# Performance work log

Hardware: AMD Instinct MI355X
Metric: run time of the kernel (lower is better)

The kernel has to match this reference:

```python
import jax, jax.numpy as jnp
import numpy as np

W_SZ = 5          # fine_window_size
D_F = 128         # fine d_model
D_C = 256         # coarse d_model


def _unfold(x, W, stride):
    # x: [B, C, H, Wd] -> [B, L, W*W, C], matching torch F.unfold + reshape/permute
    B, C, H, Wd = x.shape
    p = W // 2
    xp = jnp.pad(x, ((0, 0), (0, 0), (p, p), (p, p)))
    Hc = (H + 2 * p - W) // stride + 1
    Wc = (Wd + 2 * p - W) // stride + 1
    ri = (jnp.arange(Hc) * stride)[:, None] + jnp.arange(W)          # [Hc, W]
    ci = (jnp.arange(Wc) * stride)[:, None] + jnp.arange(W)          # [Wc, W]
    # gather -> [B, C, Hc, W, Wc, W]
    patches = xp[:, :, ri[:, :, None, None], ci[None, None, :, :]]
    # -> [B, Hc, Wc, W, W, C] -> [B, L, W*W, C]
    patches = patches.transpose(0, 2, 4, 3, 5, 1)
    return patches.reshape(B, Hc * Wc, W * W, C)


def setup_inputs() -> dict:
    key = jax.random.key(0)
    ks = jax.random.split(key, 10)
    B, Hf, Wf = 2, 240, 320
    L = 4800  # 60*80 coarse cells
    M = 3000
    inp = {
        "feat_f0": jax.random.normal(ks[0], (B, D_F, Hf, Wf), jnp.float32),
        "feat_f1": jax.random.normal(ks[1], (B, D_F, Hf, Wf), jnp.float32),
        "feat_c0": jax.random.normal(ks[2], (B, L, D_C), jnp.float32),
        "feat_c1": jax.random.normal(ks[3], (B, L, D_C), jnp.float32),
        "hw0_f": 240,
        "hw0_c": 60,
        "b_ids": jax.random.randint(ks[4], (M,), 0, B, jnp.int64 if jax.config.jax_enable_x64 else jnp.int32),
        "i_ids": jax.random.randint(ks[5], (M,), 0, L, jnp.int64 if jax.config.jax_enable_x64 else jnp.int32),
        "j_ids": jax.random.randint(ks[6], (M,), 0, L, jnp.int64 if jax.config.jax_enable_x64 else jnp.int32),
        # Linear params, torch convention: y = x @ W.T + b
        "down_W": jax.random.normal(ks[7], (D_F, D_C), jnp.float32) * (2.0 / D_C) ** 0.5,
        "down_b": jnp.zeros((D_F,), jnp.float32),
        "merge_W": jax.random.normal(ks[8], (D_F, 2 * D_F), jnp.float32) * (1.0 / D_F) ** 0.5,
        "merge_b": jnp.zeros((D_F,), jnp.float32),
    }
    return inp


def reference(feat_f0, feat_f1, feat_c0, feat_c1, hw0_f, hw0_c,
              b_ids, i_ids, j_ids, down_W, down_b, merge_W, merge_b):
    W = W_SZ
    stride = hw0_f // hw0_c  # python int -> static
    # unfold both fine maps -> [B, L, W^2, d_f]
    f0_unf = _unfold(feat_f0, W, stride)
    f1_unf = _unfold(feat_f1, W, stride)
    # gather per-match windows -> [M, W^2, d_f]
    f0_win = f0_unf[b_ids, i_ids]
    f1_win = f1_unf[b_ids, j_ids]
    # coarse feats per match, concat along match dim -> [2M, d_c]
    c_cat = jnp.concatenate([feat_c0[b_ids, i_ids], feat_c1[b_ids, j_ids]], axis=0)
    c_win = c_cat @ down_W.T + down_b                                   # [2M, d_f]
    f_cat = jnp.concatenate([f0_win, f1_win], axis=0)                   # [2M, W^2, d_f]
    c_rep = jnp.broadcast_to(c_win[:, None, :], f_cat.shape)            # [2M, W^2, d_f]
    merged = jnp.concatenate([f_cat, c_rep], axis=-1) @ merge_W.T + merge_b
    M = b_ids.shape[0]
    return merged[:M], merged[M:]
```

## Files before the change

### kernel.cpp

```cpp
#include <hip/hip_runtime.h>


#define HF 240
#define WF 320
#define HWF (HF * WF)
#define LPOS 4800

typedef short short8 __attribute__((ext_vector_type(8)));
typedef unsigned short ushort8 __attribute__((ext_vector_type(8)));
typedef float f32x4 __attribute__((ext_vector_type(4)));

__device__ __forceinline__ unsigned short f2bf(float x) {
  union { float f; unsigned u; } v; v.f = x;
  unsigned r = v.u + 0x7FFF + ((v.u >> 16) & 1);
  return (unsigned short)(r >> 16);
}

__global__ __launch_bounds__(256) void transpose_kernel(
    const float* __restrict__ f0, const float* __restrict__ f1,
    unsigned short* __restrict__ t0, unsigned short* __restrict__ t1) {
  const int t = threadIdx.x;
  const int px = blockIdx.x * 256 + t;
  const int c8 = blockIdx.y;
  const int mb = blockIdx.z;
  const float* src = ((mb >> 1) ? f1 : f0)
                   + ((size_t)(mb & 1) * 128 + (size_t)c8 * 8) * HWF + px;
  unsigned short* dst = ((mb >> 1) ? t1 : t0)
                      + (((size_t)(mb & 1) * 16 + (size_t)c8) * HWF + px) * 8;

  float v[8];
  #pragma unroll
  for (int j = 0; j < 8; ++j) v[j] = src[(size_t)j * HWF];
  ushort8 u;
  #pragma unroll
  for (int j = 0; j < 8; ++j) u[j] = f2bf(v[j]);
  *(ushort8*)dst = u;
}

__global__ __launch_bounds__(256) void prep_kernel(
    const float* __restrict__ down_W, const float* __restrict__ down_b,
    const float* __restrict__ merge_W, const float* __restrict__ merge_b,
    float* __restrict__ CW, float* __restrict__ cbias,
    unsigned short* __restrict__ W1bf) {
  int idx = blockIdx.x * 256 + threadIdx.x;
  if (idx < 32768) {
    int k = idx >> 7, o = idx & 127;
    float s = 0.f;
    #pragma unroll 4
    for (int t = 0; t < 128; ++t)
      s += down_W[t * 256 + k] * merge_W[o * 256 + 128 + t];
    CW[idx] = s;
  } else if (idx < 49152) {
    int i2 = idx - 32768;
    int n = i2 >> 7, c = i2 & 127;
    W1bf[i2] = f2bf(merge_W[n * 256 + c]);
  } else if (idx < 49280) {
    int o = idx - 49152;
    float s = merge_b[o];
    #pragma unroll 4
    for (int t = 0; t < 128; ++t)
      s += down_b[t] * merge_W[o * 256 + 128 + t];
    cbias[o] = s;
  }
}

__global__ __launch_bounds__(256) void t2_kernel(
    const float* __restrict__ c0, const float* __restrict__ c1,
    const int* __restrict__ b_ids, const int* __restrict__ i_ids,
    const int* __restrict__ j_ids,
    const float* __restrict__ CW, const float* __restrict__ cbias,
    float* __restrict__ t2, int M) {
  __shared__ float crow[8][256];
  const int t = threadIdx.x;
  const int m0 = blockIdx.x * 8;
  const int M2 = 2 * M;
  #pragma unroll
  for (int it = 0; it < 8; ++it) {
    int m = m0 + it;
    float v = 0.f;
    if (m < M2) {
      int b, pos;
      const float* src;
      if (m < M) { b = b_ids[m]; pos = i_ids[m]; src = c0; }
      else       { b = b_ids[m - M]; pos = j_ids[m - M]; src = c1; }
      v = src[((size_t)b * LPOS + pos) * 256 + t];
    }
    crow[it][t] = v;
  }
  __syncthreads();
  const int o = t & 127, half = t >> 7;
  const int r0 = half * 4;
  float a0 = 0.f, a1 = 0.f, a2 = 0.f, a3 = 0.f;
  #pragma unroll 4
  for (int k = 0; k < 256; ++k) {
    float wv = CW[k * 128 + o];
    a0 += crow[r0 + 0][k] * wv;
    a1 += crow[r0 + 1][k] * wv;
    a2 += crow[r0 + 2][k] * wv;
    a3 += crow[r0 + 3][k] * wv;
  }
  const float cb = cbias[o];
  if (m0 + r0 + 0 < M2) t2[(size_t)(m0 + r0 + 0) * 128 + o] = a0 + cb;
  if (m0 + r0 + 1 < M2) t2[(size_t)(m0 + r0 + 1) * 128 + o] = a1 + cb;
  if (m0 + r0 + 2 < M2) t2[(size_t)(m0 + r0 + 2) * 128 + o] = a2 + cb;
  if (m0 + r0 + 3 < M2) t2[(size_t)(m0 + r0 + 3) * 128 + o] = a3 + cb;
}

__global__ __launch_bounds__(256) void fine_mfma_kernel(
    const unsigned short* __restrict__ t0, const unsigned short* __restrict__ t1,
    const int* __restrict__ b_ids, const int* __restrict__ i_ids,
    const int* __restrict__ j_ids,
    const unsigned short* __restrict__ W1bf, const float* __restrict__ t2,
    float* __restrict__ out, int M) {
  __shared__ unsigned short Bl[128 * 128];
  const int t = threadIdx.x;

  #pragma unroll
  for (int it = 0; it < 8; ++it) {
    int q = it * 256 + t;
    int n = q >> 4;
    int kb16 = (q & 15) * 16;
    short8 v = *(const short8*)&W1bf[n * 128 + (q & 15) * 8];
    int dstB = n * 256 + (kb16 ^ ((n & 7) << 4));
    *(short8*)((char*)Bl + dstB) = v;
  }

  const int wid = t >> 6, lane = t & 63;
  const int lr = lane & 15, lg = lane >> 4;
  const int m = blockIdx.x * 4 + wid;
  const int M2 = 2 * M;
  const bool active = (m < M2);

  short8 a[2][4];
  short8 az = {};
  if (active) {
    int b, pos;
    const unsigned short* tm;
    if (m < M) { b = b_ids[m]; pos = i_ids[m]; tm = t0; }
    else       { int mm = m - M; b = b_ids[mm]; pos = j_ids[mm]; tm = t1; }
    tm += (size_t)b * 16 * HWF * 8;
    int hc = pos / 80, wc = pos - hc * 80;
    int h0 = hc * 4 - 2, w0 = wc * 4 - 2;
    #pragma unroll
    for (int mt = 0; mt < 2; ++mt) {
      int p = mt * 16 + lr;
      int pr = p / 5;
      int hh = h0 + pr, ww = w0 + (p - pr * 5);
      bool valid = (p < 25) && ((unsigned)hh < (unsigned)HF) && ((unsigned)ww < (unsigned)WF);
      int px = valid ? (hh * WF + ww) : 0;
      #pragma unroll
      for (int kk = 0; kk < 4; ++kk) {
        const short8* ap =
            (const short8*)(tm + (((size_t)(kk * 4 + lg) * HWF + px) << 3));
        a[mt][kk] = valid ? *ap : az;
      }
    }
  } else {
    #pragma unroll
    for (int mt = 0; mt < 2; ++mt)
      #pragma unroll
      for (int kk = 0; kk < 4; ++kk) a[mt][kk] = az;
  }

  __syncthreads();
  if (!active) return;

  f32x4 acc[2][8];
  #pragma unroll
  for (int mt = 0; mt < 2; ++mt)
    #pragma unroll
    for (int nt = 0; nt < 8; ++nt) {
      f32x4 z = {0.f, 0.f, 0.f, 0.f};
      acc[mt][nt] = z;
    }

  #pragma unroll
  for (int nt = 0; nt < 8; ++nt) {
    int n = nt * 16 + lr;
    int kbase = n * 256;
    int sw = (n & 7) << 4;
    short8 bfr[4];
    #pragma unroll
    for (int kk = 0; kk < 4; ++kk) {
      int kb = (kk * 64 + lg * 16) ^ sw;
      bfr[kk] = *(const short8*)((const char*)Bl + kbase + kb);
    }
    #pragma unroll
    for (int kk = 0; kk < 4; ++kk) {
      acc[0][nt] = __builtin_amdgcn_mfma_f32_16x16x32_bf16(a[0][kk], bfr[kk], acc[0][nt], 0, 0, 0);
      acc[1][nt] = __builtin_amdgcn_mfma_f32_16x16x32_bf16(a[1][kk], bfr[kk], acc[1][nt], 0, 0, 0);
    }
  }

  const float* t2row = t2 + (size_t)m * 128;
  float* orow = out + (size_t)m * 25 * 128;
  #pragma unroll
  for (int nt = 0; nt < 8; ++nt) {
    int o = nt * 16 + lr;
    float tv = t2row[o];
    #pragma unroll
    for (int mt = 0; mt < 2; ++mt) {
      #pragma unroll
      for (int j = 0; j < 4; ++j) {
        int r = mt * 16 + lg * 4 + j;
        if (r < 25) orow[r * 128 + o] = acc[mt][nt][j] + tv;
      }
    }
  }
}

extern "C" void kernel_launch(void* const* d_in, const int* in_sizes, int n_in,
                              void* d_out, int out_size, void* d_ws, size_t ws_size,
                              hipStream_t stream) {
  const float* f0      = (const float*)d_in[0];
  const float* f1      = (const float*)d_in[1];
  const float* c0      = (const float*)d_in[2];
  const float* c1      = (const float*)d_in[3];
  const int*   b_ids   = (const int*)d_in[6];
  const int*   i_ids   = (const int*)d_in[7];
  const int*   j_ids   = (const int*)d_in[8];
  const float* down_W  = (const float*)d_in[9];
  const float* down_b  = (const float*)d_in[10];
  const float* merge_W = (const float*)d_in[11];
  const float* merge_b = (const float*)d_in[12];
  const int M = in_sizes[6];
  const int M2 = 2 * M;

  char* wsb = (char*)d_ws;
  float* CW    = (float*)wsb;
  float* cbias = (float*)(wsb + 131072);
  float* t2    = (float*)(wsb + 131584);
  size_t off = 131584 + (size_t)M2 * 128 * 4;
  off = (off + 255) & ~(size_t)255;
  unsigned short* W1bf = (unsigned short*)(wsb + off);
  off += 32768;
  unsigned short* t0 = (unsigned short*)(wsb + off);
  off += (size_t)2 * 16 * HWF * 8 * 2;
  unsigned short* t1 = (unsigned short*)(wsb + off);

  transpose_kernel<<<dim3(300, 16, 4), 256, 0, stream>>>(f0, f1, t0, t1);
  prep_kernel<<<193, 256, 0, stream>>>(down_W, down_b, merge_W, merge_b,
                                       CW, cbias, W1bf);
  t2_kernel<<<(M2 + 7) / 8, 256, 0, stream>>>(c0, c1, b_ids, i_ids, j_ids,
                                              CW, cbias, t2, M);
  fine_mfma_kernel<<<(M2 + 3) / 4, 256, 0, stream>>>(t0, t1, b_ids, i_ids, j_ids,
                                                     W1bf, t2, (float*)d_out, M);
}
```

Measured before the change: 107.0 us.

## Gather fine windows directly from NCHW fp32 and drop the transpose pass

Removes the kernel that converted both full fine feature maps into a channel-blocked bf16 layout. The MFMA kernel now reads the 5x5 window pixels straight from the original fp32 NCHW tensors with per-channel strided loads and converts them to bf16 in registers. This avoids reading and rewriting the whole feature maps when only a small set of windows is used. In exchange, the gather is much less coalesced: each element is a scattered 4-byte load rather than a 16-byte vector load.

```diff
diff --git a/kernel.cpp b/kernel.cpp
--- a/kernel.cpp
+++ b/kernel.cpp
@@ -7,34 +7,12 @@
 #define LPOS 4800
 
 typedef short short8 __attribute__((ext_vector_type(8)));
-typedef unsigned short ushort8 __attribute__((ext_vector_type(8)));
 typedef float f32x4 __attribute__((ext_vector_type(4)));
 
 __device__ __forceinline__ unsigned short f2bf(float x) {
   union { float f; unsigned u; } v; v.f = x;
   unsigned r = v.u + 0x7FFF + ((v.u >> 16) & 1);
   return (unsigned short)(r >> 16);
-}
-
-__global__ __launch_bounds__(256) void transpose_kernel(
-    const float* __restrict__ f0, const float* __restrict__ f1,
-    unsigned short* __restrict__ t0, unsigned short* __restrict__ t1) {
-  const int t = threadIdx.x;
-  const int px = blockIdx.x * 256 + t;
-  const int c8 = blockIdx.y;
-  const int mb = blockIdx.z;
-  const float* src = ((mb >> 1) ? f1 : f0)
-                   + ((size_t)(mb & 1) * 128 + (size_t)c8 * 8) * HWF + px;
-  unsigned short* dst = ((mb >> 1) ? t1 : t0)
-                      + (((size_t)(mb & 1) * 16 + (size_t)c8) * HWF + px) * 8;
-
-  float v[8];
-  #pragma unroll
-  for (int j = 0; j < 8; ++j) v[j] = src[(size_t)j * HWF];
-  ushort8 u;
-  #pragma unroll
-  for (int j = 0; j < 8; ++j) u[j] = f2bf(v[j]);
-  *(ushort8*)dst = u;
 }
 
 __global__ __launch_bounds__(256) void prep_kernel(
@@ -107,7 +85,7 @@
 }
 
 __global__ __launch_bounds__(256) void fine_mfma_kernel(
-    const unsigned short* __restrict__ t0, const unsigned short* __restrict__ t1,
+    const float* __restrict__ f0, const float* __restrict__ f1,
     const int* __restrict__ b_ids, const int* __restrict__ i_ids,
     const int* __restrict__ j_ids,
     const unsigned short* __restrict__ W1bf, const float* __restrict__ t2,
@@ -132,13 +110,17 @@
   const bool active = (m < M2);
 
   short8 a[2][4];
-  short8 az = {};
+  #pragma unroll
+  for (int mt = 0; mt < 2; ++mt)
+    #pragma unroll
+    for (int kk = 0; kk < 4; ++kk) a[mt][kk] = (short8){};
+
   if (active) {
     int b, pos;
-    const unsigned short* tm;
-    if (m < M) { b = b_ids[m]; pos = i_ids[m]; tm = t0; }
-    else       { int mm = m - M; b = b_ids[mm]; pos = j_ids[mm]; tm = t1; }
-    tm += (size_t)b * 16 * HWF * 8;
+    const float* src;
+    if (m < M) { b = b_ids[m]; pos = i_ids[m]; src = f0; }
+    else       { int mm = m - M; b = b_ids[mm]; pos = j_ids[mm]; src = f1; }
+    const float* base = src + (size_t)b * 128 * HWF;
     int hc = pos / 80, wc = pos - hc * 80;
     int h0 = hc * 4 - 2, w0 = wc * 4 - 2;
     #pragma unroll
@@ -147,19 +129,19 @@
       int pr = p / 5;
       int hh = h0 + pr, ww = w0 + (p - pr * 5);
       bool valid = (p < 25) && ((unsigned)hh < (unsigned)HF) && ((unsigned)ww < (unsigned)WF);
-      int px = valid ? (hh * WF + ww) : 0;
+      const float* ap = base + (valid ? (hh * WF + ww) : 0) + (size_t)lg * 8 * HWF;
       #pragma unroll
       for (int kk = 0; kk < 4; ++kk) {
-        const short8* ap =
-            (const short8*)(tm + (((size_t)(kk * 4 + lg) * HWF + px) << 3));
-        a[mt][kk] = valid ? *ap : az;
+        float v[8];
+        #pragma unroll
+        for (int j = 0; j < 8; ++j)
+          v[j] = valid ? ap[((size_t)kk * 32 + j) * HWF] : 0.f;
+        short8 fr;
+        #pragma unroll
+        for (int j = 0; j < 8; ++j) fr[j] = (short)f2bf(v[j]);
+        a[mt][kk] = fr;
       }
     }
-  } else {
-    #pragma unroll
-    for (int mt = 0; mt < 2; ++mt)
-      #pragma unroll
-      for (int kk = 0; kk < 4; ++kk) a[mt][kk] = az;
   }
 
   __syncthreads();
@@ -233,16 +215,11 @@
   size_t off = 131584 + (size_t)M2 * 128 * 4;
   off = (off + 255) & ~(size_t)255;
   unsigned short* W1bf = (unsigned short*)(wsb + off);
-  off += 32768;
-  unsigned short* t0 = (unsigned short*)(wsb + off);
-  off += (size_t)2 * 16 * HWF * 8 * 2;
-  unsigned short* t1 = (unsigned short*)(wsb + off);
-
-  transpose_kernel<<<dim3(300, 16, 4), 256, 0, stream>>>(f0, f1, t0, t1);
+
   prep_kernel<<<193, 256, 0, stream>>>(down_W, down_b, merge_W, merge_b,
                                        CW, cbias, W1bf);
   t2_kernel<<<(M2 + 7) / 8, 256, 0, stream>>>(c0, c1, b_ids, i_ids, j_ids,
                                               CW, cbias, t2, M);
-  fine_mfma_kernel<<<(M2 + 3) / 4, 256, 0, stream>>>(t0, t1, b_ids, i_ids, j_ids,
+  fine_mfma_kernel<<<(M2 + 3) / 4, 256, 0, stream>>>(f0, f1, b_ids, i_ids, j_ids,
                                                      W1bf, t2, (float*)d_out, M);
 }
```

Result: slower. 143.0 us (+33.6%).

## Merge transpose into t2 kernel and process two matches per wave in MFMA kernel

Applied to the files above, without the earlier changes.

The fp32-to-bf16 channel-packing transpose now runs as extra blocks of the t2 projection kernel, which removes one launch and lets the two independent jobs overlap. The transposed output is written with nontemporal stores. The fine MFMA kernel now loops over two matches per wave, so each staged copy of the bf16 weight in shared memory is reused across eight matches instead of four. The cost is a serial loop inside each wave and half as many blocks, which lowers parallelism and latency hiding for the gather loads.

```diff
diff --git a/kernel.cpp b/kernel.cpp
--- a/kernel.cpp
+++ b/kernel.cpp
@@ -14,27 +14,6 @@
   union { float f; unsigned u; } v; v.f = x;
   unsigned r = v.u + 0x7FFF + ((v.u >> 16) & 1);
   return (unsigned short)(r >> 16);
-}
-
-__global__ __launch_bounds__(256) void transpose_kernel(
-    const float* __restrict__ f0, const float* __restrict__ f1,
-    unsigned short* __restrict__ t0, unsigned short* __restrict__ t1) {
-  const int t = threadIdx.x;
-  const int px = blockIdx.x * 256 + t;
-  const int c8 = blockIdx.y;
-  const int mb = blockIdx.z;
-  const float* src = ((mb >> 1) ? f1 : f0)
-                   + ((size_t)(mb & 1) * 128 + (size_t)c8 * 8) * HWF + px;
-  unsigned short* dst = ((mb >> 1) ? t1 : t0)
-                      + (((size_t)(mb & 1) * 16 + (size_t)c8) * HWF + px) * 8;
-
-  float v[8];
-  #pragma unroll
-  for (int j = 0; j < 8; ++j) v[j] = src[(size_t)j * HWF];
-  ushort8 u;
-  #pragma unroll
-  for (int j = 0; j < 8; ++j) u[j] = f2bf(v[j]);
-  *(ushort8*)dst = u;
 }
 
 __global__ __launch_bounds__(256) void prep_kernel(
@@ -64,15 +43,39 @@
   }
 }
 
-__global__ __launch_bounds__(256) void t2_kernel(
+__global__ __launch_bounds__(256) void work_kernel(
+    const float* __restrict__ f0, const float* __restrict__ f1,
+    unsigned short* __restrict__ t0, unsigned short* __restrict__ t1,
     const float* __restrict__ c0, const float* __restrict__ c1,
     const int* __restrict__ b_ids, const int* __restrict__ i_ids,
     const int* __restrict__ j_ids,
     const float* __restrict__ CW, const float* __restrict__ cbias,
-    float* __restrict__ t2, int M) {
+    float* __restrict__ t2, int M, int T2B) {
   __shared__ float crow[8][256];
   const int t = threadIdx.x;
-  const int m0 = blockIdx.x * 8;
+  const int bid = blockIdx.x;
+
+  if (bid >= T2B) {
+    const int q = bid - T2B;
+    const int bx = q % 300;
+    const int c8 = (q / 300) & 15;
+    const int mb = q / 4800;
+    const int px = bx * 256 + t;
+    const float* src = ((mb >> 1) ? f1 : f0)
+                     + ((size_t)(mb & 1) * 128 + (size_t)c8 * 8) * HWF + px;
+    unsigned short* dst = ((mb >> 1) ? t1 : t0)
+                        + (((size_t)(mb & 1) * 16 + (size_t)c8) * HWF + px) * 8;
+    float v[8];
+    #pragma unroll
+    for (int j = 0; j < 8; ++j) v[j] = src[(size_t)j * HWF];
+    ushort8 u;
+    #pragma unroll
+    for (int j = 0; j < 8; ++j) u[j] = f2bf(v[j]);
+    __builtin_nontemporal_store(u, (ushort8*)dst);
+    return;
+  }
+
+  const int m0 = bid * 8;
   const int M2 = 2 * M;
   #pragma unroll
   for (int it = 0; it < 8; ++it) {
@@ -124,86 +127,83 @@
     int dstB = n * 256 + (kb16 ^ ((n & 7) << 4));
     *(short8*)((char*)Bl + dstB) = v;
   }
+  __syncthreads();
 
   const int wid = t >> 6, lane = t & 63;
   const int lr = lane & 15, lg = lane >> 4;
-  const int m = blockIdx.x * 4 + wid;
   const int M2 = 2 * M;
-  const bool active = (m < M2);
-
-  short8 a[2][4];
-  short8 az = {};
-  if (active) {
-    int b, pos;
-    const unsigned short* tm;
-    if (m < M) { b = b_ids[m]; pos = i_ids[m]; tm = t0; }
-    else       { int mm = m - M; b = b_ids[mm]; pos = j_ids[mm]; tm = t1; }
-    tm += (size_t)b * 16 * HWF * 8;
-    int hc = pos / 80, wc = pos - hc * 80;
-    int h0 = hc * 4 - 2, w0 = wc * 4 - 2;
-    #pragma unroll
-    for (int mt = 0; mt < 2; ++mt) {
-      int p = mt * 16 + lr;
-      int pr = p / 5;
-      int hh = h0 + pr, ww = w0 + (p - pr * 5);
-      bool valid = (p < 25) && ((unsigned)hh < (unsigned)HF) && ((unsigned)ww < (unsigned)WF);
-      int px = valid ? (hh * WF + ww) : 0;
+
+  #pragma unroll 1
+  for (int im = 0; im < 2; ++im) {
+    const int m = blockIdx.x * 8 + im * 4 + wid;
+    if (m >= M2) continue;
+
+    short8 a[2][4];
+    short8 az = {};
+    {
+      int b, pos;
+      const unsigned short* tm;
+      if (m < M) { b = b_ids[m]; pos = i_ids[m]; tm = t0; }
+      else       { int mm = m - M; b = b_ids[mm]; pos = j_ids[mm]; tm = t1; }
+      tm += (size_t)b * 16 * HWF * 8;
+      int hc = pos / 80, wc = pos - hc * 80;
+      int h0 = hc * 4 - 2, w0 = wc * 4 - 2;
+      #pragma unroll
+      for (int mt = 0; mt < 2; ++mt) {
+        int p = mt * 16 + lr;
+        int pr = p / 5;
+        int hh = h0 + pr, ww = w0 + (p - pr * 5);
+        bool valid = (p < 25) && ((unsigned)hh < (unsigned)HF) && ((unsigned)ww < (unsigned)WF);
+        int px = valid ? (hh * WF + ww) : 0;
+        #pragma unroll
+        for (int kk = 0; kk < 4; ++kk) {
+          const short8* ap =
+              (const short8*)(tm + (((size_t)(kk * 4 + lg) * HWF + px) << 3));
+          a[mt][kk] = valid ? *ap : az;
+        }
+      }
+    }
+
+    f32x4 acc[2][8];
+    #pragma unroll
+    for (int mt = 0; mt < 2; ++mt)
+      #pragma unroll
+      for (int nt = 0; nt < 8; ++nt) {
+        f32x4 z = {0.f, 0.f, 0.f, 0.f};
+        acc[mt][nt] = z;
+      }
+
+    #pragma unroll
+    for (int nt = 0; nt < 8; ++nt) {
+      int n = nt * 16 + lr;
+      int kbase = n * 256;
+      int sw = (n & 7) << 4;
+      short8 bfr[4];
       #pragma unroll
       for (int kk = 0; kk < 4; ++kk) {
-        const short8* ap =
-            (const short8*)(tm + (((size_t)(kk * 4 + lg) * HWF + px) << 3));
-        a[mt][kk] = valid ? *ap : az;
-      }
-    }
-  } else {
-    #pragma unroll
-    for (int mt = 0; mt < 2; ++mt)
-      #pragma unroll
-      for (int kk = 0; kk < 4; ++kk) a[mt][kk] = az;
-  }
-
-  __syncthreads();
-  if (!active) return;
-
-  f32x4 acc[2][8];
-  #pragma unroll
-  for (int mt = 0; mt < 2; ++mt)
+        int kb = (kk * 64 + lg * 16) ^ sw;
+        bfr[kk] = *(const short8*)((const char*)Bl + kbase + kb);
+      }
+      #pragma unroll
+      for (int kk = 0; kk < 4; ++kk) {
+        acc[0][nt] = __builtin_amdgcn_mfma_f32_16x16x32_bf16(a[0][kk], bfr[kk], acc[0][nt], 0, 0, 0);
+        acc[1][nt] = __builtin_amdgcn_mfma_f32_16x16x32_bf16(a[1][kk], bfr[kk], acc[1][nt], 0, 0, 0);
+      }
+    }
+
+    const float* t2row = t2 + (size_t)m * 128;
+    float* orow = out + (size_t)m * 25 * 128;
     #pragma unroll
     for (int nt = 0; nt < 8; ++nt) {
-      f32x4 z = {0.f, 0.f, 0.f, 0.f};
-      acc[mt][nt] = z;
-    }
-
-  #pragma unroll
-  for (int nt = 0; nt < 8; ++nt) {
-    int n = nt * 16 + lr;
-    int kbase = n * 256;
-    int sw = (n & 7) << 4;
-    short8 bfr[4];
-    #pragma unroll
-    for (int kk = 0; kk < 4; ++kk) {
-      int kb = (kk * 64 + lg * 16) ^ sw;
-      bfr[kk] = *(const short8*)((const char*)Bl + kbase + kb);
-    }
-    #pragma unroll
-    for (int kk = 0; kk < 4; ++kk) {
-      acc[0][nt] = __builtin_amdgcn_mfma_f32_16x16x32_bf16(a[0][kk], bfr[kk], acc[0][nt], 0, 0, 0);
-      acc[1][nt] = __builtin_amdgcn_mfma_f32_16x16x32_bf16(a[1][kk], bfr[kk], acc[1][nt], 0, 0, 0);
-    }
-  }
-
-  const float* t2row = t2 + (size_t)m * 128;
-  float* orow = out + (size_t)m * 25 * 128;
-  #pragma unroll
-  for (int nt = 0; nt < 8; ++nt) {
-    int o = nt * 16 + lr;
-    float tv = t2row[o];
-    #pragma unroll
-    for (int mt = 0; mt < 2; ++mt) {
-      #pragma unroll
-      for (int j = 0; j < 4; ++j) {
-        int r = mt * 16 + lg * 4 + j;
-        if (r < 25) orow[r * 128 + o] = acc[mt][nt][j] + tv;
+      int o = nt * 16 + lr;
+      float tv = t2row[o];
+      #pragma unroll
+      for (int mt = 0; mt < 2; ++mt) {
+        #pragma unroll
+        for (int j = 0; j < 4; ++j) {
+          int r = mt * 16 + lg * 4 + j;
+          if (r < 25) orow[r * 128 + o] = acc[mt][nt][j] + tv;
+        }
       }
     }
   }
@@ -225,6 +225,7 @@
   const float* merge_b = (const float*)d_in[12];
   const int M = in_sizes[6];
   const int M2 = 2 * M;
+  const int T2B = (M2 + 7) / 8;
 
   char* wsb = (char*)d_ws;
   float* CW    = (float*)wsb;
@@ -238,11 +239,11 @@
   off += (size_t)2 * 16 * HWF * 8 * 2;
   unsigned short* t1 = (unsigned short*)(wsb + off);
 
-  transpose_kernel<<<dim3(300, 16, 4), 256, 0, stream>>>(f0, f1, t0, t1);
   prep_kernel<<<193, 256, 0, stream>>>(down_W, down_b, merge_W, merge_b,
                                        CW, cbias, W1bf);
-  t2_kernel<<<(M2 + 7) / 8, 256, 0, stream>>>(c0, c1, b_ids, i_ids, j_ids,
-                                              CW, cbias, t2, M);
-  fine_mfma_kernel<<<(M2 + 3) / 4, 256, 0, stream>>>(t0, t1, b_ids, i_ids, j_ids,
+  work_kernel<<<T2B + 19200, 256, 0, stream>>>(f0, f1, t0, t1, c0, c1,
+                                               b_ids, i_ids, j_ids,
+                                               CW, cbias, t2, M, T2B);
+  fine_mfma_kernel<<<(M2 + 7) / 8, 256, 0, stream>>>(t0, t1, b_ids, i_ids, j_ids,
                                                      W1bf, t2, (float*)d_out, M);
 }
```

After: 99.23 us (median of 2 runs). 1.08x faster.

## Fuse coarse projection into fine MFMA kernel and use nontemporal transpose stores

Applied to the files above, without the earlier changes.

Merges the coarse-feature projection (t2) kernel into the fine MFMA kernel. Each block now handles 8 matches, computes their projected coarse rows into shared memory, then each wave processes two matches in sequence. This removes one kernel launch and the global round trip of the t2 buffer, and spreads the W1 shared-memory load over twice as many matches. The transpose kernel now uses nontemporal stores and is launched after prep. The cost is more shared memory per block and half as many blocks, with serialized work inside each wave.

```diff
diff --git a/kernel.cpp b/kernel.cpp
--- a/kernel.cpp
+++ b/kernel.cpp
@@ -34,7 +34,7 @@
   ushort8 u;
   #pragma unroll
   for (int j = 0; j < 8; ++j) u[j] = f2bf(v[j]);
-  *(ushort8*)dst = u;
+  __builtin_nontemporal_store(u, (ushort8*)dst);
 }
 
 __global__ __launch_bounds__(256) void prep_kernel(
@@ -64,56 +64,19 @@
   }
 }
 
-__global__ __launch_bounds__(256) void t2_kernel(
+__global__ __launch_bounds__(256) void fine_mfma_kernel(
+    const unsigned short* __restrict__ t0, const unsigned short* __restrict__ t1,
     const float* __restrict__ c0, const float* __restrict__ c1,
     const int* __restrict__ b_ids, const int* __restrict__ i_ids,
     const int* __restrict__ j_ids,
+    const unsigned short* __restrict__ W1bf,
     const float* __restrict__ CW, const float* __restrict__ cbias,
-    float* __restrict__ t2, int M) {
-  __shared__ float crow[8][256];
-  const int t = threadIdx.x;
-  const int m0 = blockIdx.x * 8;
-  const int M2 = 2 * M;
-  #pragma unroll
-  for (int it = 0; it < 8; ++it) {
-    int m = m0 + it;
-    float v = 0.f;
-    if (m < M2) {
-      int b, pos;
-      const float* src;
-      if (m < M) { b = b_ids[m]; pos = i_ids[m]; src = c0; }
-      else       { b = b_ids[m - M]; pos = j_ids[m - M]; src = c1; }
-      v = src[((size_t)b * LPOS + pos) * 256 + t];
-    }
-    crow[it][t] = v;
-  }
-  __syncthreads();
-  const int o = t & 127, half = t >> 7;
-  const int r0 = half * 4;
-  float a0 = 0.f, a1 = 0.f, a2 = 0.f, a3 = 0.f;
-  #pragma unroll 4
-  for (int k = 0; k < 256; ++k) {
-    float wv = CW[k * 128 + o];
-    a0 += crow[r0 + 0][k] * wv;
-    a1 += crow[r0 + 1][k] * wv;
-    a2 += crow[r0 + 2][k] * wv;
-    a3 += crow[r0 + 3][k] * wv;
-  }
-  const float cb = cbias[o];
-  if (m0 + r0 + 0 < M2) t2[(size_t)(m0 + r0 + 0) * 128 + o] = a0 + cb;
-  if (m0 + r0 + 1 < M2) t2[(size_t)(m0 + r0 + 1) * 128 + o] = a1 + cb;
-  if (m0 + r0 + 2 < M2) t2[(size_t)(m0 + r0 + 2) * 128 + o] = a2 + cb;
-  if (m0 + r0 + 3 < M2) t2[(size_t)(m0 + r0 + 3) * 128 + o] = a3 + cb;
-}
-
-__global__ __launch_bounds__(256) void fine_mfma_kernel(
-    const unsigned short* __restrict__ t0, const unsigned short* __restrict__ t1,
-    const int* __restrict__ b_ids, const int* __restrict__ i_ids,
-    const int* __restrict__ j_ids,
-    const unsigned short* __restrict__ W1bf, const float* __restrict__ t2,
     float* __restrict__ out, int M) {
   __shared__ unsigned short Bl[128 * 128];
+  __shared__ float crow[8][256];
+  __shared__ float t2l[8][128];
   const int t = threadIdx.x;
+  const int M2 = 2 * M;
 
   #pragma unroll
   for (int it = 0; it < 8; ++it) {
@@ -125,85 +88,116 @@
     *(short8*)((char*)Bl + dstB) = v;
   }
 
+  const int m0 = blockIdx.x * 8;
+  #pragma unroll
+  for (int it = 0; it < 8; ++it) {
+    int m = m0 + it;
+    float v = 0.f;
+    if (m < M2) {
+      int b, pos;
+      const float* srcc;
+      if (m < M) { b = b_ids[m]; pos = i_ids[m]; srcc = c0; }
+      else       { b = b_ids[m - M]; pos = j_ids[m - M]; srcc = c1; }
+      v = srcc[((size_t)b * LPOS + pos) * 256 + t];
+    }
+    crow[it][t] = v;
+  }
+  __syncthreads();
+
+  {
+    const int o = t & 127, half = t >> 7;
+    const int r0 = half * 4;
+    float a0 = 0.f, a1 = 0.f, a2 = 0.f, a3 = 0.f;
+    #pragma unroll 4
+    for (int k = 0; k < 256; ++k) {
+      float wv = CW[k * 128 + o];
+      a0 += crow[r0 + 0][k] * wv;
+      a1 += crow[r0 + 1][k] * wv;
+      a2 += crow[r0 + 2][k] * wv;
+      a3 += crow[r0 + 3][k] * wv;
+    }
+    const float cb = cbias[o];
+    t2l[r0 + 0][o] = a0 + cb;
+    t2l[r0 + 1][o] = a1 + cb;
+    t2l[r0 + 2][o] = a2 + cb;
+    t2l[r0 + 3][o] = a3 + cb;
+  }
+  __syncthreads();
+
   const int wid = t >> 6, lane = t & 63;
   const int lr = lane & 15, lg = lane >> 4;
-  const int m = blockIdx.x * 4 + wid;
-  const int M2 = 2 * M;
-  const bool active = (m < M2);
-
-  short8 a[2][4];
-  short8 az = {};
-  if (active) {
-    int b, pos;
-    const unsigned short* tm;
-    if (m < M) { b = b_ids[m]; pos = i_ids[m]; tm = t0; }
-    else       { int mm = m - M; b = b_ids[mm]; pos = j_ids[mm]; tm = t1; }
-    tm += (size_t)b * 16 * HWF * 8;
-    int hc = pos / 80, wc = pos - hc * 80;
-    int h0 = hc * 4 - 2, w0 = wc * 4 - 2;
-    #pragma unroll
-    for (int mt = 0; mt < 2; ++mt) {
-      int p = mt * 16 + lr;
-      int pr = p / 5;
-      int hh = h0 + pr, ww = w0 + (p - pr * 5);
-      bool valid = (p < 25) && ((unsigned)hh < (unsigned)HF) && ((unsigned)ww < (unsigned)WF);
-      int px = valid ? (hh * WF + ww) : 0;
-      #pragma unroll
-      for (int kk = 0; kk < 4; ++kk) {
-        const short8* ap =
-            (const short8*)(tm + (((size_t)(kk * 4 + lg) * HWF + px) << 3));
-        a[mt][kk] = valid ? *ap : az;
-      }
-    }
-  } else {
+
+  #pragma unroll 1
+  for (int im = 0; im < 2; ++im) {
+    const int mrow = im * 4 + wid;
+    const int m = m0 + mrow;
+    if (m >= M2) continue;
+
+    short8 a[2][4];
+    short8 az = {};
+    {
+      int b, pos;
+      const unsigned short* tm;
+      if (m < M) { b = b_ids[m]; pos = i_ids[m]; tm = t0; }
+      else       { int mm = m - M; b = b_ids[mm]; pos = j_ids[mm]; tm = t1; }
+      tm += (size_t)b * 16 * HWF * 8;
+      int hc = pos / 80, wc = pos - hc * 80;
+      int h0 = hc * 4 - 2, w0 = wc * 4 - 2;
+      #pragma unroll
+      for (int mt = 0; mt < 2; ++mt) {
+        int p = mt * 16 + lr;
+        int pr = p / 5;
+        int hh = h0 + pr, ww = w0 + (p - pr * 5);
+        bool valid = (p < 25) && ((unsigned)hh < (unsigned)HF) && ((unsigned)ww < (unsigned)WF);
+        int px = valid ? (hh * WF + ww) : 0;
+        #pragma unroll
+        for (int kk = 0; kk < 4; ++kk) {
+          const short8* ap =
+              (const short8*)(tm + (((size_t)(kk * 4 + lg) * HWF + px) << 3));
+          a[mt][kk] = valid ? *ap : az;
+        }
+      }
+    }
+
+    f32x4 acc[2][8];
     #pragma unroll
     for (int mt = 0; mt < 2; ++mt)
       #pragma unroll
-      for (int kk = 0; kk < 4; ++kk) a[mt][kk] = az;
-  }
-
-  __syncthreads();
-  if (!active) return;
-
-  f32x4 acc[2][8];
-  #pragma unroll
-  for (int mt = 0; mt < 2; ++mt)
+      for (int nt = 0; nt < 8; ++nt) {
+        f32x4 z = {0.f, 0.f, 0.f, 0.f};
+        acc[mt][nt] = z;
+      }
+
     #pragma unroll
     for (int nt = 0; nt < 8; ++nt) {
-      f32x4 z = {0.f, 0.f, 0.f, 0.f};
-      acc[mt][nt] = z;
-    }
-
-  #pragma unroll
-  for (int nt = 0; nt < 8; ++nt) {
-    int n = nt * 16 + lr;
-    int kbase = n * 256;
-    int sw = (n & 7) << 4;
-    short8 bfr[4];
+      int n = nt * 16 + lr;
+      int kbase = n * 256;
+      int sw = (n & 7) << 4;
+      short8 bfr[4];
+      #pragma unroll
+      for (int kk = 0; kk < 4; ++kk) {
+        int kb = (kk * 64 + lg * 16) ^ sw;
+        bfr[kk] = *(const short8*)((const char*)Bl + kbase + kb);
+      }
+      #pragma unroll
+      for (int kk = 0; kk < 4; ++kk) {
+        acc[0][nt] = __builtin_amdgcn_mfma_f32_16x16x32_bf16(a[0][kk], bfr[kk], acc[0][nt], 0, 0, 0);
+        acc[1][nt] = __builtin_amdgcn_mfma_f32_16x16x32_bf16(a[1][kk], bfr[kk], acc[1][nt], 0, 0, 0);
+      }
+    }
+
+    float* orow = out + (size_t)m * 25 * 128;
     #pragma unroll
-    for (int kk = 0; kk < 4; ++kk) {
-      int kb = (kk * 64 + lg * 16) ^ sw;
-      bfr[kk] = *(const short8*)((const char*)Bl + kbase + kb);
-    }
-    #pragma unroll
-    for (int kk = 0; kk < 4; ++kk) {
-      acc[0][nt] = __builtin_amdgcn_mfma_f32_16x16x32_bf16(a[0][kk], bfr[kk], acc[0][nt], 0, 0, 0);
-      acc[1][nt] = __builtin_amdgcn_mfma_f32_16x16x32_bf16(a[1][kk], bfr[kk], acc[1][nt], 0, 0, 0);
-    }
-  }
-
-  const float* t2row = t2 + (size_t)m * 128;
-  float* orow = out + (size_t)m * 25 * 128;
-  #pragma unroll
-  for (int nt = 0; nt < 8; ++nt) {
-    int o = nt * 16 + lr;
-    float tv = t2row[o];
-    #pragma unroll
-    for (int mt = 0; mt < 2; ++mt) {
-      #pragma unroll
-      for (int j = 0; j < 4; ++j) {
-        int r = mt * 16 + lg * 4 + j;
-        if (r < 25) orow[r * 128 + o] = acc[mt][nt][j] + tv;
+    for (int nt = 0; nt < 8; ++nt) {
+      int o = nt * 16 + lr;
+      float tv = t2l[mrow][o];
+      #pragma unroll
+      for (int mt = 0; mt < 2; ++mt) {
+        #pragma unroll
+        for (int j = 0; j < 4; ++j) {
+          int r = mt * 16 + lg * 4 + j;
+          if (r < 25) orow[r * 128 + o] = acc[mt][nt][j] + tv;
+        }
       }
     }
   }
@@ -229,8 +223,7 @@
   char* wsb = (char*)d_ws;
   float* CW    = (float*)wsb;
   float* cbias = (float*)(wsb + 131072);
-  float* t2    = (float*)(wsb + 131584);
-  size_t off = 131584 + (size_t)M2 * 128 * 4;
+  size_t off = 131584;
   off = (off + 255) & ~(size_t)255;
   unsigned short* W1bf = (unsigned short*)(wsb + off);
   off += 32768;
@@ -238,11 +231,11 @@
   off += (size_t)2 * 16 * HWF * 8 * 2;
   unsigned short* t1 = (unsigned short*)(wsb + off);
 
-  transpose_kernel<<<dim3(300, 16, 4), 256, 0, stream>>>(f0, f1, t0, t1);
   prep_kernel<<<193, 256, 0, stream>>>(down_W, down_b, merge_W, merge_b,
                                        CW, cbias, W1bf);
-  t2_kernel<<<(M2 + 7) / 8, 256, 0, stream>>>(c0, c1, b_ids, i_ids, j_ids,
-                                              CW, cbias, t2, M);
-  fine_mfma_kernel<<<(M2 + 3) / 4, 256, 0, stream>>>(t0, t1, b_ids, i_ids, j_ids,
-                                                     W1bf, t2, (float*)d_out, M);
-}
+  transpose_kernel<<<dim3(300, 16, 4), 256, 0, stream>>>(f0, f1, t0, t1);
+  fine_mfma_kernel<<<(M2 + 7) / 8, 256, 0, stream>>>(t0, t1, c0, c1,
+                                                     b_ids, i_ids, j_ids,
+                                                     W1bf, CW, cbias,
+                                                     (float*)d_out, M);
+}
```

Measured after the change: 104.8 us. 2.0% less time.
